# Performance work log

Measured on AMD Instinct MI355X. Metric: run time of the kernel, lower is better.

Reference implementation:

```python
import jax, jax.numpy as jnp
import numpy as np

H = 512; W = 512          # image size
K = 1024                  # fixed cap on points per cloud (original is data-dependent)
P = 8                     # n_points = n_points_rate * radius
R = 1.0                   # radius
THR = 5                   # point_threshould
LAM = 0.1                 # lam


def _lbp_uniform(img):
    """skimage-style uniform LBP, P=8, R=1, bilinear sampling (edge-clamped)."""
    Hh, Ww = img.shape
    rows = jnp.arange(Hh)
    cols = jnp.arange(Ww)
    bits = []
    for k in range(P):
        dr = float(np.round(-R * np.sin(2.0 * np.pi * k / P), 8))
        dc = float(np.round(R * np.cos(2.0 * np.pi * k / P), 8))
        rr = rows + dr
        cc = cols + dc
        r0 = jnp.floor(rr)
        c0 = jnp.floor(cc)
        fr = (rr - r0)[:, None]
        fc = (cc - c0)[None, :]
        r0i = jnp.clip(r0.astype(jnp.int32), 0, Hh - 1)
        r1i = jnp.clip(r0i + 1, 0, Hh - 1)
        c0i = jnp.clip(c0.astype(jnp.int32), 0, Ww - 1)
        c1i = jnp.clip(c0i + 1, 0, Ww - 1)
        g = lambda ri, ci: img[ri][:, ci]
        sample = ((1 - fr) * ((1 - fc) * g(r0i, c0i) + fc * g(r0i, c1i))
                  + fr * ((1 - fc) * g(r1i, c0i) + fc * g(r1i, c1i)))
        bits.append((sample - img >= 0).astype(jnp.int32))
    b = jnp.stack(bits)                                    # [P,H,W]
    changes = jnp.sum(jnp.abs(b - jnp.roll(b, 1, axis=0)), axis=0)
    s = jnp.sum(b, axis=0)
    return jnp.where(changes <= 2, s, P + 1).astype(jnp.float32)


def _select_points(mask2d):
    """Row-major coordinates of True pixels, zero-padded/truncated to K points."""
    flat = mask2d.reshape(-1)
    order = jnp.argsort(jnp.where(flat, 0, 1), stable=True)[:K]  # True pixels first, row-major
    valid = flat[order].astype(jnp.float32)
    r = (order // W).astype(jnp.float32)
    c = (order % W).astype(jnp.float32)
    return jnp.stack([r, c], axis=-1) * valid[:, None]     # [K,2]


def _pdist(x):
    sq = jnp.sum(x * x, axis=-1)
    d2 = sq[:, None] + sq[None, :] - 2.0 * (x @ x.T)
    return jnp.sqrt(jnp.maximum(d2, 0.0))


def _mst_pairing(D):
    """Prim's MST edges = dim-0 Vietoris-Rips persistence pairing. [K-1,2] int32."""
    N = D.shape[0]
    INF = jnp.float32(1e9)
    in_tree = jnp.zeros(N, bool).at[0].set(True)
    mind = D[0]
    src = jnp.zeros(N, jnp.int32)

    def step(carry, _):
        mind, src, in_tree = carry
        j = jnp.argmin(jnp.where(in_tree, INF, mind)).astype(jnp.int32)
        edge = jnp.stack([src[j], j])
        in_tree = in_tree.at[j].set(True)
        upd = (D[j] < mind) & ~in_tree
        mind = jnp.where(upd, D[j], mind)
        src = jnp.where(upd, j, src)
        return (mind, src, in_tree), edge

    _, edges = jax.lax.scan(step, (mind, src, in_tree), None, length=N - 1)
    return edges


def _sample_loss(pred_bin, mask_bin):
    pts_p = _select_points(_lbp_uniform(pred_bin) < THR)
    pts_m = _select_points(_lbp_uniform(mask_bin) < THR)
    Dp = _pdist(pts_p)
    Dm = _pdist(pts_m)
    ep = _mst_pairing(Dp)
    em = _mst_pairing(Dm)
    sig = lambda D, e: D[e[:, 0], e[:, 1]]
    l_p = jnp.linalg.norm(sig(Dp, ep) - sig(Dm, ep))   # signature of pred pairing
    l_m = jnp.linalg.norm(sig(Dp, em) - sig(Dm, em))   # signature of mask pairing
    return l_p + l_m


def setup_inputs() -> dict:
    key = jax.random.key(0)
    k1, k2, k3 = jax.random.split(key, 3)
    images = jax.random.normal(k1, (8, 1, H, W), dtype=jnp.float32)
    model_output = jax.random.normal(k2, (8, 1, H, W), dtype=jnp.float32)
    labels = jax.random.uniform(k3, (8, 1, H, W), dtype=jnp.float32)
    return {"images": images, "model_output": model_output, "labels": labels}


def reference(images, model_output, labels):
    preds = jax.nn.sigmoid(model_output[:, 0])          # squeeze channel dim
    masks = labels[:, 0]
    pred_bin = (preds > 0.5).astype(jnp.float32)
    mask_bin = (masks > 0.5).astype(jnp.float32)
    per_sample = jax.vmap(_sample_loss)(pred_bin, mask_bin)
    return LAM * jnp.sum(per_sample) / pred_bin.shape[0]
```

## Files before the change

kernel.cpp:

```cpp
#include <hip/hip_runtime.h>

#define HH 512
#define WW 512
#define NPIX (HH * WW)
#define NIMG 16
#define KPTS 1024
#define NWORDS (NPIX / 64)

__global__ void lbp_kernel(const float* __restrict__ mo,
                           const float* __restrict__ lb,
                           unsigned long long* __restrict__ maskbits) {
    int m = blockIdx.y;
    int pix = blockIdx.x * blockDim.x + threadIdx.x;
    int r = pix >> 9, c = pix & 511;
    int sample = m >> 1;
    const float* img = (m & 1) ? (lb + sample * NPIX) : (mo + sample * NPIX);
    float thr = (m & 1) ? 0.5f : 0.0f;

    int rm = r - (r > 0), rp = r + (r < HH - 1);
    int cm = c - (c > 0), cp = c + (c < WW - 1);
    const float* rowm = img + rm * WW;
    const float* row0 = img + r  * WW;
    const float* rowp = img + rp * WW;

    bool bmm = rowm[cm] > thr, bm0 = rowm[c] > thr, bmp = rowm[cp] > thr;
    bool b0m = row0[cm] > thr, b00 = row0[c] > thr, b0p = row0[cp] > thr;
    bool bpm = rowp[cm] > thr, bp0 = rowp[c] > thr, bpp = rowp[cp] > thr;

    bool r0e = (r == 0), c0e = (c == 0);
    bool t2m = r0e ? bpm : b0m;
    bool t2c = r0e ? bp0 : b00;
    bool t2p = r0e ? bpp : b0p;
    bool mc2 = c0e ? bmp : bm0;
    bool tc2 = c0e ? t2p : t2c;
    bool zc2 = c0e ? b0p : b00;
    bool pc2 = c0e ? bpp : bp0;

    unsigned bb =
        (b0p                     ?   1u : 0u)
      | ((bm0 & bmp & t2c & t2p) ?   2u : 0u)
      | (bm0                     ?   4u : 0u)
      | ((bmm & mc2 & t2m & tc2) ?   8u : 0u)
      | (b0m                     ?  16u : 0u)
      | ((b0m & zc2 & bpm & pc2) ?  32u : 0u)
      | (bp0                     ?  64u : 0u)
      | ((b0p & bp0 & bpp)       ? 128u : 0u);

    unsigned rol = ((bb << 1) | (bb >> 7)) & 0xFFu;
    int changes = __popc(bb ^ rol);
    int s = __popc(bb);
    bool maskbit = b00 && (changes <= 2) && (s < 5);

    unsigned long long w = __ballot(maskbit);
    if ((threadIdx.x & 63) == 0)
        maskbits[m * NWORDS + (pix >> 6)] = w;
}

__global__ void select_kernel(const unsigned long long* __restrict__ maskbits,
                              unsigned* __restrict__ ptsG) {
    __shared__ unsigned swv[4];
    int m = blockIdx.x, tid = threadIdx.x;
    int lane = tid & 63, wid = tid >> 6;

    for (int i = tid; i < KPTS; i += 256) ptsG[m * KPTS + i] = 0u;
    __syncthreads();

    unsigned running = 0;
    for (int ch = 0; ch < 16; ch++) {
        int w = ch * 256 + tid;
        unsigned long long word = maskbits[m * NWORDS + w];
        unsigned cnt = (unsigned)__popcll(word);

        unsigned x = cnt;
#pragma unroll
        for (int d = 1; d < 64; d <<= 1) {
            unsigned y = (unsigned)__shfl_up((int)x, d, 64);
            x += (lane >= d) ? y : 0u;
        }
        if (lane == 63) swv[wid] = x;
        __syncthreads();
        unsigned woff = 0, total = 0;
#pragma unroll
        for (int ww = 0; ww < 4; ww++) {
            unsigned t = swv[ww];
            total += t;
            woff += (ww < wid) ? t : 0u;
        }
        unsigned rank = running + woff + x - cnt;
        while (word) {
            int b = __builtin_ctzll(word);
            word &= word - 1;
            if (rank < (unsigned)KPTS) {
                unsigned p = (unsigned)(w * 64 + b);
                unsigned rr = p >> 9, cc = p & 511u;
                ptsG[m * KPTS + rank] = (rr << 16) | cc;
            }
            rank++;
        }
        running += total;
        if (running >= (unsigned)KPTS) break;
        __syncthreads();
    }
}

typedef short v2s __attribute__((ext_vector_type(2)));

__device__ __forceinline__ int dist2_packed(unsigned a, unsigned b) {
#if __has_builtin(__builtin_amdgcn_sdot2)
    v2s d = __builtin_bit_cast(v2s, a) - __builtin_bit_cast(v2s, b);
    return __builtin_amdgcn_sdot2(d, d, 0, false);
#else
    int dr = (int)(a >> 16) - (int)(b >> 16);
    int dc = (int)(a & 0xFFFFu) - (int)(b & 0xFFFFu);
    return __mul24(dr, dr) + __mul24(dc, dc);
#endif
}

template <int CTRL>
__device__ __forceinline__ unsigned umin_dpp(unsigned x) {
    unsigned o = (unsigned)__builtin_amdgcn_update_dpp((int)x, (int)x, CTRL,
                                                       0xf, 0xf, false);
    return o < x ? o : x;
}

__device__ __forceinline__ unsigned umin3(unsigned a, unsigned b, unsigned c) {
    unsigned t = a < b ? a : b;
    return t < c ? t : c;
}

__device__ __forceinline__ unsigned mk_key(unsigned ps, unsigned qs, int izb) {
#if __has_builtin(__builtin_amdgcn_sdot2)
    v2s d = __builtin_bit_cast(v2s, ps) - __builtin_bit_cast(v2s, qs);
    return (unsigned)__builtin_amdgcn_sdot2(d, d, izb, false);
#else
    int dr = (int)(short)(ps >> 16) - (int)(short)(qs >> 16);
    int dc = (int)(short)(ps & 0xFFFFu) - (int)(short)(qs & 0xFFFFu);
    return (unsigned)(dr * dr + dc * dc + izb);
#endif
}

#define SLOT_INIT(s, ps, ks, iz)                                          \
    iz = ((s << 6) | lane) - 1024;             \
    ps = base[(s << 6) | lane] << 5;             \
    ks = mk_key(ps, pt0s, iz);

#define SLOT_UPD(s, ps, ks, iz)                                           \
    { unsigned _nk = mk_key(ps, pjs, iz);                                 \
      ks = (unsigned)min((int)ks, (int)_nk); }

#define INLANE_MIN16(res)                                                 \
    { unsigned _m0 = umin3(k0, k1, k2);                                   \
      unsigned _m1 = umin3(k3, k4, k5);                                   \
      unsigned _m2 = umin3(k6, k7, k8);                                   \
      unsigned _m3 = umin3(k9, k10, k11);                                 \
      unsigned _m4 = umin3(k12, k13, k14);                                \
      unsigned _ra = umin3(_m0, _m1, _m2);                                \
      unsigned _rb = umin3(_m3, _m4, k15);                                \
      res = _ra < _rb ? _ra : _rb; }

#define SEL16P(res)                                                       \
    { unsigned _a0 = b0 ? p1  : p0;                                       \
      unsigned _a1 = b0 ? p3  : p2;                                       \
      unsigned _a2 = b0 ? p5  : p4;                                       \
      unsigned _a3 = b0 ? p7  : p6;                                       \
      unsigned _a4 = b0 ? p9  : p8;                                       \
      unsigned _a5 = b0 ? p11 : p10;                                      \
      unsigned _a6 = b0 ? p13 : p12;                                      \
      unsigned _a7 = b0 ? p15 : p14;                                      \
      unsigned _c0 = b1 ? _a1 : _a0;                                      \
      unsigned _c1 = b1 ? _a3 : _a2;                                      \
      unsigned _c2 = b1 ? _a5 : _a4;                                      \
      unsigned _c3 = b1 ? _a7 : _a6;                                      \
      unsigned _e0 = b2 ? _c1 : _c0;                                      \
      unsigned _e1 = b2 ? _c3 : _c2;                                      \
      res = b3 ? _e1 : _e0; }

#define PIN16(P) asm volatile("" :                                        \
    "+v"(P##0), "+v"(P##1), "+v"(P##2),  "+v"(P##3),                      \
    "+v"(P##4), "+v"(P##5), "+v"(P##6),  "+v"(P##7),                      \
    "+v"(P##8), "+v"(P##9), "+v"(P##10), "+v"(P##11),                     \
    "+v"(P##12), "+v"(P##13), "+v"(P##14), "+v"(P##15))

__global__ __launch_bounds__(64, 1) void mst_kernel(const unsigned* __restrict__ ptsG,
                                                    unsigned* __restrict__ edgesG) {
    int lane = threadIdx.x;
    int m = blockIdx.x;
    const unsigned* base = ptsG + m * KPTS;
    unsigned pt0s = base[0] << 5;

    unsigned k0,k1,k2,k3,k4,k5,k6,k7,k8,k9,k10,k11,k12,k13,k14,k15;
    unsigned p0,p1,p2,p3,p4,p5,p6,p7,p8,p9,p10,p11,p12,p13,p14,p15;
    int      i0,i1,i2,i3,i4,i5,i6,i7,i8,i9,i10,i11,i12,i13,i14,i15;

    SLOT_INIT(0,  p0,  k0,  i0);   SLOT_INIT(1,  p1,  k1,  i1);
    SLOT_INIT(2,  p2,  k2,  i2);   SLOT_INIT(3,  p3,  k3,  i3);
    SLOT_INIT(4,  p4,  k4,  i4);   SLOT_INIT(5,  p5,  k5,  i5);
    SLOT_INIT(6,  p6,  k6,  i6);   SLOT_INIT(7,  p7,  k7,  i7);
    SLOT_INIT(8,  p8,  k8,  i8);   SLOT_INIT(9,  p9,  k9,  i9);
    SLOT_INIT(10, p10, k10, i10);  SLOT_INIT(11, p11, k11, i11);
    SLOT_INIT(12, p12, k12, i12);  SLOT_INIT(13, p13, k13, i13);
    SLOT_INIT(14, p14, k14, i14);  SLOT_INIT(15, p15, k15, i15);

    unsigned* eout = edgesG + m * KPTS;
    unsigned rk;
    INLANE_MIN16(rk);

    unsigned acc = 0;

    for (int chk = 0; chk < 16; chk++) {
        int tmax = (chk < 15) ? 64 : 63;
        for (int t = 0; t < tmax; t++) {
            PIN16(p); PIN16(k);

            rk = umin_dpp<0x111>(rk);
            rk = umin_dpp<0x112>(rk);
            rk = umin_dpp<0x114>(rk);
            rk = umin_dpp<0x118>(rk);
            unsigned q0 = (unsigned)__builtin_amdgcn_readlane((int)rk, 15);
            unsigned q1 = (unsigned)__builtin_amdgcn_readlane((int)rk, 31);
            unsigned q2 = (unsigned)__builtin_amdgcn_readlane((int)rk, 47);
            unsigned q3 = (unsigned)__builtin_amdgcn_readlane((int)rk, 63);
            unsigned wa = q0 < q1 ? q0 : q1;
            unsigned wb = q2 < q3 ? q2 : q3;
            unsigned wk = (wa < wb ? wa : wb) + 1024u;

            unsigned j = wk & 1023u;
            int wslot = (int)(j >> 6);
            int wlane = (int)(j & 63u);

            bool b0 = (wslot & 1) != 0, b1 = (wslot & 2) != 0;
            bool b2 = (wslot & 4) != 0, b3 = (wslot & 8) != 0;
            unsigned selPay;
            SEL16P(selPay);
            unsigned pjs = (unsigned)__builtin_amdgcn_readlane((int)selPay, wlane);

            acc = (lane == t) ? wk : acc;

            SLOT_UPD(0,  p0,  k0,  i0);   SLOT_UPD(1,  p1,  k1,  i1);
            SLOT_UPD(2,  p2,  k2,  i2);   SLOT_UPD(3,  p3,  k3,  i3);
            SLOT_UPD(4,  p4,  k4,  i4);   SLOT_UPD(5,  p5,  k5,  i5);
            SLOT_UPD(6,  p6,  k6,  i6);   SLOT_UPD(7,  p7,  k7,  i7);
            SLOT_UPD(8,  p8,  k8,  i8);   SLOT_UPD(9,  p9,  k9,  i9);
            SLOT_UPD(10, p10, k10, i10);  SLOT_UPD(11, p11, k11, i11);
            SLOT_UPD(12, p12, k12, i12);  SLOT_UPD(13, p13, k13, i13);
            SLOT_UPD(14, p14, k14, i14);  SLOT_UPD(15, p15, k15, i15);

            INLANE_MIN16(rk);
        }
        eout[(chk << 6) + lane] = acc;
    }
}

__global__ void recover_kernel(const unsigned* __restrict__ ptsG,
                               const unsigned* __restrict__ edgesG,
                               float* __restrict__ contrib) {
    __shared__ unsigned sS[KPTS];
    __shared__ unsigned sO[KPTS];
    __shared__ unsigned short sT[KPTS];
    int g = blockIdx.x, m = blockIdx.y;
    int tid = threadIdx.x;
    int partner = m ^ 1;

    for (int i = tid; i < KPTS; i += 256) {
        sS[i] = ptsG[m * KPTS + i];
        sO[i] = ptsG[partner * KPTS + i];
    }
    for (int e = tid; e < KPTS - 1; e += 256) {
        unsigned wkk = edgesG[m * KPTS + e];
        sT[wkk & 1023u] = (unsigned short)(e + 1);
    }
    if (tid == 0) sT[0] = 0;
    __syncthreads();

    int lane = tid & 63, w = tid >> 6;
    for (int k = 0; k < 16; k++) {
        int e = g * 64 + w * 16 + k;
        if (e >= KPTS - 1) break;
        unsigned wk = edgesG[m * KPTS + e];
        unsigned j = wk & 1023u;
        unsigned d2p = wk >> 10;
        unsigned pj = sS[j];
        unsigned te1 = (unsigned)(e + 1);

        unsigned best = 0xFFFFFFFFu;
#pragma unroll
        for (int i = 0; i < 16; i++) {
            int v = i * 64 + lane;
            unsigned pv = sS[v];
            int d2 = dist2_packed(pv, pj);
            unsigned tv1 = (unsigned)sT[v];
            bool qual = ((unsigned)d2 == d2p) && (tv1 < te1);
            unsigned cand = qual ? ((tv1 << 10) | (unsigned)v) : 0xFFFFFFFFu;
            best = cand < best ? cand : best;
        }
#pragma unroll
        for (int dd = 32; dd; dd >>= 1) {
            unsigned o = (unsigned)__shfl_xor((int)best, dd, 64);
            best = o < best ? o : best;
        }
        unsigned vsrc = best & 1023u;
        if (lane == 0) {
            unsigned oj = sO[j], os = sO[vsrc];
            float Dp = __fsqrt_rn((float)d2p);
            float Dm = __fsqrt_rn((float)dist2_packed(oj, os));
            float diff = Dp - Dm;
            contrib[m * (KPTS - 1) + e] = diff * diff;
        }
    }
}

__global__ void final_kernel(const float* __restrict__ contrib,
                             float* __restrict__ out) {
    __shared__ double part[NIMG];
    int t = threadIdx.x;
    if (t < NIMG) {
        double s = 0.0;
        for (int e = 0; e < KPTS - 1; e++)
            s += (double)contrib[t * (KPTS - 1) + e];
        part[t] = sqrt(s);
    }
    __syncthreads();
    if (t == 0) {
        double tot = 0.0;
        for (int i = 0; i < NIMG; i++) tot += part[i];
        out[0] = (float)(0.1 * tot / 8.0);
    }
}

extern "C" void kernel_launch(void* const* d_in, const int* in_sizes, int n_in,
                              void* d_out, int out_size, void* d_ws, size_t ws_size,
                              hipStream_t stream) {
    const float* mo = (const float*)d_in[1];
    const float* lb = (const float*)d_in[2];

    unsigned long long* maskbits = (unsigned long long*)d_ws;
    unsigned* edgesG = (unsigned*)d_ws;
    float* contrib = (float*)((char*)d_ws + (size_t)64 * 1024);
    unsigned* ptsG = (unsigned*)((char*)d_ws + (size_t)NIMG * NWORDS * 8);
    float* out = (float*)d_out;

    lbp_kernel<<<dim3(NPIX / 256, NIMG), 256, 0, stream>>>(mo, lb, maskbits);
    select_kernel<<<NIMG, 256, 0, stream>>>(maskbits, ptsG);
    mst_kernel<<<NIMG, 64, 0, stream>>>(ptsG, edgesG);
    recover_kernel<<<dim3(16, NIMG), 256, 0, stream>>>(ptsG, edgesG, contrib);
    final_kernel<<<1, 64, 0, stream>>>(contrib, out);
}
```

Before: 435.1 us.

## Split Prim MST update across four waves with LDS cross-wave min

The Prim MST kernel now runs each cloud with 256 threads (four waves) instead of one wave. Each wave owns 4 of the 16 key slots, reduces them to lane 63 with DPP, and publishes the result to a double-buffered shared array; after a barrier every wave reads the four partials and takes the global min. Every wave still holds all 16 point payloads so it can look up the winner locally. This shortens the per-iteration distance-update work per wave, at the cost of a __syncthreads and an LDS round trip on each of the 1023 serial steps.

```diff
diff --git a/kernel.cpp b/kernel.cpp
--- a/kernel.cpp
+++ b/kernel.cpp
@@ -104,6 +104,7 @@
 }
 
 typedef short v2s __attribute__((ext_vector_type(2)));
+typedef unsigned u32x4 __attribute__((ext_vector_type(4)));
 
 __device__ __forceinline__ int dist2_packed(unsigned a, unsigned b) {
 #if __has_builtin(__builtin_amdgcn_sdot2)
@@ -123,6 +124,16 @@
     return o < x ? o : x;
 }
 
+__device__ __forceinline__ unsigned wave_min_to_lane63(unsigned x) {
+    x = umin_dpp<0x111>(x);
+    x = umin_dpp<0x112>(x);
+    x = umin_dpp<0x114>(x);
+    x = umin_dpp<0x118>(x);
+    x = umin_dpp<0x142>(x);
+    x = umin_dpp<0x143>(x);
+    return x;
+}
+
 __device__ __forceinline__ unsigned umin3(unsigned a, unsigned b, unsigned c) {
     unsigned t = a < b ? a : b;
     return t < c ? t : c;
@@ -139,24 +150,14 @@
 #endif
 }
 
-#define SLOT_INIT(s, ps, ks, iz)                                          \
-    iz = ((s << 6) | lane) - 1024;             \
-    ps = base[(s << 6) | lane] << 5;             \
-    ks = mk_key(ps, pt0s, iz);
-
-#define SLOT_UPD(s, ps, ks, iz)                                           \
-    { unsigned _nk = mk_key(ps, pjs, iz);                                 \
-      ks = (unsigned)min((int)ks, (int)_nk); }
-
-#define INLANE_MIN16(res)                                                 \
-    { unsigned _m0 = umin3(k0, k1, k2);                                   \
-      unsigned _m1 = umin3(k3, k4, k5);                                   \
-      unsigned _m2 = umin3(k6, k7, k8);                                   \
-      unsigned _m3 = umin3(k9, k10, k11);                                 \
-      unsigned _m4 = umin3(k12, k13, k14);                                \
-      unsigned _ra = umin3(_m0, _m1, _m2);                                \
-      unsigned _rb = umin3(_m3, _m4, k15);                                \
-      res = _ra < _rb ? _ra : _rb; }
+#define OSLOT_INIT(sl)                                                    \
+    oi##sl = (((wid * 4 + sl) << 6) | lane) - 1024;       \
+    oq##sl = base[((wid * 4 + sl) << 6) | lane] << 5;                     \
+    ok##sl = mk_key(oq##sl, pt0s, oi##sl);
+
+#define OSLOT_UPD(sl)                                                     \
+    { unsigned _nk = mk_key(oq##sl, pjs, oi##sl);                         \
+      ok##sl = (unsigned)min((int)ok##sl, (int)_nk); }
 
 #define SEL16P(res)                                                       \
     { unsigned _a0 = b0 ? p1  : p0;                                       \
@@ -175,54 +176,56 @@
       unsigned _e1 = b2 ? _c3 : _c2;                                      \
       res = b3 ? _e1 : _e0; }
 
-#define PIN16(P) asm volatile("" :                                        \
-    "+v"(P##0), "+v"(P##1), "+v"(P##2),  "+v"(P##3),                      \
-    "+v"(P##4), "+v"(P##5), "+v"(P##6),  "+v"(P##7),                      \
-    "+v"(P##8), "+v"(P##9), "+v"(P##10), "+v"(P##11),                     \
-    "+v"(P##12), "+v"(P##13), "+v"(P##14), "+v"(P##15))
-
-__global__ __launch_bounds__(64, 1) void mst_kernel(const unsigned* __restrict__ ptsG,
-                                                    unsigned* __restrict__ edgesG) {
-    int lane = threadIdx.x;
+__global__ __launch_bounds__(256, 1) void mst_kernel(const unsigned* __restrict__ ptsG,
+                                                     unsigned* __restrict__ edgesG) {
+    __shared__ __align__(16) unsigned xmin[2][4];
+    int tid = threadIdx.x;
+    int lane = tid & 63, wid = tid >> 6;
     int m = blockIdx.x;
     const unsigned* base = ptsG + m * KPTS;
     unsigned pt0s = base[0] << 5;
 
-    unsigned k0,k1,k2,k3,k4,k5,k6,k7,k8,k9,k10,k11,k12,k13,k14,k15;
-    unsigned p0,p1,p2,p3,p4,p5,p6,p7,p8,p9,p10,p11,p12,p13,p14,p15;
-    int      i0,i1,i2,i3,i4,i5,i6,i7,i8,i9,i10,i11,i12,i13,i14,i15;
-
-    SLOT_INIT(0,  p0,  k0,  i0);   SLOT_INIT(1,  p1,  k1,  i1);
-    SLOT_INIT(2,  p2,  k2,  i2);   SLOT_INIT(3,  p3,  k3,  i3);
-    SLOT_INIT(4,  p4,  k4,  i4);   SLOT_INIT(5,  p5,  k5,  i5);
-    SLOT_INIT(6,  p6,  k6,  i6);   SLOT_INIT(7,  p7,  k7,  i7);
-    SLOT_INIT(8,  p8,  k8,  i8);   SLOT_INIT(9,  p9,  k9,  i9);
-    SLOT_INIT(10, p10, k10, i10);  SLOT_INIT(11, p11, k11, i11);
-    SLOT_INIT(12, p12, k12, i12);  SLOT_INIT(13, p13, k13, i13);
-    SLOT_INIT(14, p14, k14, i14);  SLOT_INIT(15, p15, k15, i15);
+    unsigned p0  = base[( 0 << 6) | lane] << 5;
+    unsigned p1  = base[( 1 << 6) | lane] << 5;
+    unsigned p2  = base[( 2 << 6) | lane] << 5;
+    unsigned p3  = base[( 3 << 6) | lane] << 5;
+    unsigned p4  = base[( 4 << 6) | lane] << 5;
+    unsigned p5  = base[( 5 << 6) | lane] << 5;
+    unsigned p6  = base[( 6 << 6) | lane] << 5;
+    unsigned p7  = base[( 7 << 6) | lane] << 5;
+    unsigned p8  = base[( 8 << 6) | lane] << 5;
+    unsigned p9  = base[( 9 << 6) | lane] << 5;
+    unsigned p10 = base[(10 << 6) | lane] << 5;
+    unsigned p11 = base[(11 << 6) | lane] << 5;
+    unsigned p12 = base[(12 << 6) | lane] << 5;
+    unsigned p13 = base[(13 << 6) | lane] << 5;
+    unsigned p14 = base[(14 << 6) | lane] << 5;
+    unsigned p15 = base[(15 << 6) | lane] << 5;
+
+    unsigned oq0, oq1, oq2, oq3;
+    unsigned ok0, ok1, ok2, ok3;
+    int      oi0, oi1, oi2, oi3;
+    OSLOT_INIT(0); OSLOT_INIT(1); OSLOT_INIT(2); OSLOT_INIT(3);
 
     unsigned* eout = edgesG + m * KPTS;
-    unsigned rk;
-    INLANE_MIN16(rk);
+    unsigned r3i = umin3(ok0, ok1, ok2);
+    unsigned rk = r3i < ok3 ? r3i : ok3;
 
     unsigned acc = 0;
+    int par = 0;
 
     for (int chk = 0; chk < 16; chk++) {
         int tmax = (chk < 15) ? 64 : 63;
         for (int t = 0; t < tmax; t++) {
-            PIN16(p); PIN16(k);
-
-            rk = umin_dpp<0x111>(rk);
-            rk = umin_dpp<0x112>(rk);
-            rk = umin_dpp<0x114>(rk);
-            rk = umin_dpp<0x118>(rk);
-            unsigned q0 = (unsigned)__builtin_amdgcn_readlane((int)rk, 15);
-            unsigned q1 = (unsigned)__builtin_amdgcn_readlane((int)rk, 31);
-            unsigned q2 = (unsigned)__builtin_amdgcn_readlane((int)rk, 47);
-            unsigned q3 = (unsigned)__builtin_amdgcn_readlane((int)rk, 63);
-            unsigned wa = q0 < q1 ? q0 : q1;
-            unsigned wb = q2 < q3 ? q2 : q3;
-            unsigned wk = (wa < wb ? wa : wb) + 1024u;
+            unsigned wmin = wave_min_to_lane63(rk);
+            if (lane == 63) xmin[par][wid] = wmin;
+            __syncthreads();
+
+            u32x4 xv = *reinterpret_cast<const u32x4*>(&xmin[par][0]);
+            unsigned vm = umin3(xv.x, xv.y, xv.z);
+            vm = vm < xv.w ? vm : xv.w;
+            unsigned wk = (unsigned)__builtin_amdgcn_readfirstlane((int)vm) + 1024u;
+            par ^= 1;
 
             unsigned j = wk & 1023u;
             int wslot = (int)(j >> 6);
@@ -236,18 +239,11 @@
 
             acc = (lane == t) ? wk : acc;
 
-            SLOT_UPD(0,  p0,  k0,  i0);   SLOT_UPD(1,  p1,  k1,  i1);
-            SLOT_UPD(2,  p2,  k2,  i2);   SLOT_UPD(3,  p3,  k3,  i3);
-            SLOT_UPD(4,  p4,  k4,  i4);   SLOT_UPD(5,  p5,  k5,  i5);
-            SLOT_UPD(6,  p6,  k6,  i6);   SLOT_UPD(7,  p7,  k7,  i7);
-            SLOT_UPD(8,  p8,  k8,  i8);   SLOT_UPD(9,  p9,  k9,  i9);
-            SLOT_UPD(10, p10, k10, i10);  SLOT_UPD(11, p11, k11, i11);
-            SLOT_UPD(12, p12, k12, i12);  SLOT_UPD(13, p13, k13, i13);
-            SLOT_UPD(14, p14, k14, i14);  SLOT_UPD(15, p15, k15, i15);
-
-            INLANE_MIN16(rk);
-        }
-        eout[(chk << 6) + lane] = acc;
+            OSLOT_UPD(0); OSLOT_UPD(1); OSLOT_UPD(2); OSLOT_UPD(3);
+            unsigned r3 = umin3(ok0, ok1, ok2);
+            rk = r3 < ok3 ? r3 : ok3;
+        }
+        if (wid == 0) eout[(chk << 6) + lane] = acc;
     }
 }
 
@@ -341,7 +337,7 @@
 
     lbp_kernel<<<dim3(NPIX / 256, NIMG), 256, 0, stream>>>(mo, lb, maskbits);
     select_kernel<<<NIMG, 256, 0, stream>>>(maskbits, ptsG);
-    mst_kernel<<<NIMG, 64, 0, stream>>>(ptsG, edgesG);
+    mst_kernel<<<NIMG, 256, 0, stream>>>(ptsG, edgesG);
     recover_kernel<<<dim3(16, NIMG), 256, 0, stream>>>(ptsG, edgesG, contrib);
     final_kernel<<<1, 64, 0, stream>>>(contrib, out);
 }
```

New measurement: 412.2 us. -5.3%, faster.

## Interleave two independent Prim MST chains per wavefront to hide latency

Applied to the files above, without the earlier changes.

The MST kernel now processes two point clouds per 64-lane wavefront, interleaving their serial Prim iterations so the DPP reductions, readlanes and key updates of one chain can fill the latency gaps of the other. The grid is halved from 16 to 8 blocks, and the asm register pins are dropped in favour of unroll-1 loops. This trades fewer busy CUs and twice the registers per wave for more instruction-level parallelism in a latency-bound serial loop.

```diff
diff --git a/kernel.cpp b/kernel.cpp
--- a/kernel.cpp
+++ b/kernel.cpp
@@ -116,16 +116,16 @@
 #endif
 }
 
+__device__ __forceinline__ unsigned umin3(unsigned a, unsigned b, unsigned c) {
+    unsigned t = a < b ? a : b;
+    return t < c ? t : c;
+}
+
 template <int CTRL>
 __device__ __forceinline__ unsigned umin_dpp(unsigned x) {
     unsigned o = (unsigned)__builtin_amdgcn_update_dpp((int)x, (int)x, CTRL,
                                                        0xf, 0xf, false);
     return o < x ? o : x;
-}
-
-__device__ __forceinline__ unsigned umin3(unsigned a, unsigned b, unsigned c) {
-    unsigned t = a < b ? a : b;
-    return t < c ? t : c;
 }
 
 __device__ __forceinline__ unsigned mk_key(unsigned ps, unsigned qs, int izb) {
@@ -139,115 +139,126 @@
 #endif
 }
 
-#define SLOT_INIT(s, ps, ks, iz)                                          \
-    iz = ((s << 6) | lane) - 1024;             \
-    ps = base[(s << 6) | lane] << 5;             \
-    ks = mk_key(ps, pt0s, iz);
-
-#define SLOT_UPD(s, ps, ks, iz)                                           \
-    { unsigned _nk = mk_key(ps, pjs, iz);                                 \
-      ks = (unsigned)min((int)ks, (int)_nk); }
-
-#define INLANE_MIN16(res)                                                 \
-    { unsigned _m0 = umin3(k0, k1, k2);                                   \
-      unsigned _m1 = umin3(k3, k4, k5);                                   \
-      unsigned _m2 = umin3(k6, k7, k8);                                   \
-      unsigned _m3 = umin3(k9, k10, k11);                                 \
-      unsigned _m4 = umin3(k12, k13, k14);                                \
+#define SEL16B(P, B0, B1, B2, B3, res)                                    \
+    { unsigned _a0 = B0 ? P##1  : P##0;                                   \
+      unsigned _a1 = B0 ? P##3  : P##2;                                   \
+      unsigned _a2 = B0 ? P##5  : P##4;                                   \
+      unsigned _a3 = B0 ? P##7  : P##6;                                   \
+      unsigned _a4 = B0 ? P##9  : P##8;                                   \
+      unsigned _a5 = B0 ? P##11 : P##10;                                  \
+      unsigned _a6 = B0 ? P##13 : P##12;                                  \
+      unsigned _a7 = B0 ? P##15 : P##14;                                  \
+      unsigned _c0 = B1 ? _a1 : _a0;                                      \
+      unsigned _c1 = B1 ? _a3 : _a2;                                      \
+      unsigned _c2 = B1 ? _a5 : _a4;                                      \
+      unsigned _c3 = B1 ? _a7 : _a6;                                      \
+      unsigned _e0 = B2 ? _c1 : _c0;                                      \
+      unsigned _e1 = B2 ? _c3 : _c2;                                      \
+      res = B3 ? _e1 : _e0; }
+
+#define SLOT_INIT2(s)                                                     \
+    iz##s = ((s << 6) | lane) - 1024;                                     \
+    pX##s = baseX[(s << 6) | lane] << 5;                                  \
+    kX##s = mk_key(pX##s, pt0sX, iz##s);                                  \
+    pY##s = baseY[(s << 6) | lane] << 5;                                  \
+    kY##s = mk_key(pY##s, pt0sY, iz##s);
+
+#define UPD2(s)                                                           \
+    { unsigned _nX = mk_key(pX##s, pjsX, iz##s);                          \
+      kX##s = (unsigned)min((int)kX##s, (int)_nX);                        \
+      unsigned _nY = mk_key(pY##s, pjsY, iz##s);                          \
+      kY##s = (unsigned)min((int)kY##s, (int)_nY); }
+
+#define MIN16(K, res)                                                     \
+    { unsigned _m0 = umin3(K##0, K##1, K##2);                             \
+      unsigned _m1 = umin3(K##3, K##4, K##5);                             \
+      unsigned _m2 = umin3(K##6, K##7, K##8);                             \
+      unsigned _m3 = umin3(K##9, K##10, K##11);                           \
+      unsigned _m4 = umin3(K##12, K##13, K##14);                          \
       unsigned _ra = umin3(_m0, _m1, _m2);                                \
-      unsigned _rb = umin3(_m3, _m4, k15);                                \
+      unsigned _rb = umin3(_m3, _m4, K##15);                              \
       res = _ra < _rb ? _ra : _rb; }
-
-#define SEL16P(res)                                                       \
-    { unsigned _a0 = b0 ? p1  : p0;                                       \
-      unsigned _a1 = b0 ? p3  : p2;                                       \
-      unsigned _a2 = b0 ? p5  : p4;                                       \
-      unsigned _a3 = b0 ? p7  : p6;                                       \
-      unsigned _a4 = b0 ? p9  : p8;                                       \
-      unsigned _a5 = b0 ? p11 : p10;                                      \
-      unsigned _a6 = b0 ? p13 : p12;                                      \
-      unsigned _a7 = b0 ? p15 : p14;                                      \
-      unsigned _c0 = b1 ? _a1 : _a0;                                      \
-      unsigned _c1 = b1 ? _a3 : _a2;                                      \
-      unsigned _c2 = b1 ? _a5 : _a4;                                      \
-      unsigned _c3 = b1 ? _a7 : _a6;                                      \
-      unsigned _e0 = b2 ? _c1 : _c0;                                      \
-      unsigned _e1 = b2 ? _c3 : _c2;                                      \
-      res = b3 ? _e1 : _e0; }
-
-#define PIN16(P) asm volatile("" :                                        \
-    "+v"(P##0), "+v"(P##1), "+v"(P##2),  "+v"(P##3),                      \
-    "+v"(P##4), "+v"(P##5), "+v"(P##6),  "+v"(P##7),                      \
-    "+v"(P##8), "+v"(P##9), "+v"(P##10), "+v"(P##11),                     \
-    "+v"(P##12), "+v"(P##13), "+v"(P##14), "+v"(P##15))
 
 __global__ __launch_bounds__(64, 1) void mst_kernel(const unsigned* __restrict__ ptsG,
                                                     unsigned* __restrict__ edgesG) {
     int lane = threadIdx.x;
-    int m = blockIdx.x;
-    const unsigned* base = ptsG + m * KPTS;
-    unsigned pt0s = base[0] << 5;
-
-    unsigned k0,k1,k2,k3,k4,k5,k6,k7,k8,k9,k10,k11,k12,k13,k14,k15;
-    unsigned p0,p1,p2,p3,p4,p5,p6,p7,p8,p9,p10,p11,p12,p13,p14,p15;
-    int      i0,i1,i2,i3,i4,i5,i6,i7,i8,i9,i10,i11,i12,i13,i14,i15;
-
-    SLOT_INIT(0,  p0,  k0,  i0);   SLOT_INIT(1,  p1,  k1,  i1);
-    SLOT_INIT(2,  p2,  k2,  i2);   SLOT_INIT(3,  p3,  k3,  i3);
-    SLOT_INIT(4,  p4,  k4,  i4);   SLOT_INIT(5,  p5,  k5,  i5);
-    SLOT_INIT(6,  p6,  k6,  i6);   SLOT_INIT(7,  p7,  k7,  i7);
-    SLOT_INIT(8,  p8,  k8,  i8);   SLOT_INIT(9,  p9,  k9,  i9);
-    SLOT_INIT(10, p10, k10, i10);  SLOT_INIT(11, p11, k11, i11);
-    SLOT_INIT(12, p12, k12, i12);  SLOT_INIT(13, p13, k13, i13);
-    SLOT_INIT(14, p14, k14, i14);  SLOT_INIT(15, p15, k15, i15);
-
-    unsigned* eout = edgesG + m * KPTS;
-    unsigned rk;
-    INLANE_MIN16(rk);
-
-    unsigned acc = 0;
-
+    int b = blockIdx.x;
+    const unsigned* baseX = ptsG + (2 * b)     * KPTS;
+    const unsigned* baseY = ptsG + (2 * b + 1) * KPTS;
+    unsigned pt0sX = baseX[0] << 5;
+    unsigned pt0sY = baseY[0] << 5;
+
+    unsigned pX0,pX1,pX2,pX3,pX4,pX5,pX6,pX7,pX8,pX9,pX10,pX11,pX12,pX13,pX14,pX15;
+    unsigned pY0,pY1,pY2,pY3,pY4,pY5,pY6,pY7,pY8,pY9,pY10,pY11,pY12,pY13,pY14,pY15;
+    unsigned kX0,kX1,kX2,kX3,kX4,kX5,kX6,kX7,kX8,kX9,kX10,kX11,kX12,kX13,kX14,kX15;
+    unsigned kY0,kY1,kY2,kY3,kY4,kY5,kY6,kY7,kY8,kY9,kY10,kY11,kY12,kY13,kY14,kY15;
+    int      iz0,iz1,iz2,iz3,iz4,iz5,iz6,iz7,iz8,iz9,iz10,iz11,iz12,iz13,iz14,iz15;
+
+    SLOT_INIT2(0)  SLOT_INIT2(1)  SLOT_INIT2(2)  SLOT_INIT2(3)
+    SLOT_INIT2(4)  SLOT_INIT2(5)  SLOT_INIT2(6)  SLOT_INIT2(7)
+    SLOT_INIT2(8)  SLOT_INIT2(9)  SLOT_INIT2(10) SLOT_INIT2(11)
+    SLOT_INIT2(12) SLOT_INIT2(13) SLOT_INIT2(14) SLOT_INIT2(15)
+
+    unsigned* eoutX = edgesG + (2 * b)     * KPTS;
+    unsigned* eoutY = edgesG + (2 * b + 1) * KPTS;
+
+    unsigned rX, rY;
+    MIN16(kX, rX);
+    MIN16(kY, rY);
+
+    unsigned accX = 0, accY = 0;
+
+#pragma unroll 1
     for (int chk = 0; chk < 16; chk++) {
         int tmax = (chk < 15) ? 64 : 63;
+#pragma unroll 1
         for (int t = 0; t < tmax; t++) {
-            PIN16(p); PIN16(k);
-
-            rk = umin_dpp<0x111>(rk);
-            rk = umin_dpp<0x112>(rk);
-            rk = umin_dpp<0x114>(rk);
-            rk = umin_dpp<0x118>(rk);
-            unsigned q0 = (unsigned)__builtin_amdgcn_readlane((int)rk, 15);
-            unsigned q1 = (unsigned)__builtin_amdgcn_readlane((int)rk, 31);
-            unsigned q2 = (unsigned)__builtin_amdgcn_readlane((int)rk, 47);
-            unsigned q3 = (unsigned)__builtin_amdgcn_readlane((int)rk, 63);
-            unsigned wa = q0 < q1 ? q0 : q1;
-            unsigned wb = q2 < q3 ? q2 : q3;
-            unsigned wk = (wa < wb ? wa : wb) + 1024u;
-
-            unsigned j = wk & 1023u;
-            int wslot = (int)(j >> 6);
-            int wlane = (int)(j & 63u);
-
-            bool b0 = (wslot & 1) != 0, b1 = (wslot & 2) != 0;
-            bool b2 = (wslot & 4) != 0, b3 = (wslot & 8) != 0;
-            unsigned selPay;
-            SEL16P(selPay);
-            unsigned pjs = (unsigned)__builtin_amdgcn_readlane((int)selPay, wlane);
-
-            acc = (lane == t) ? wk : acc;
-
-            SLOT_UPD(0,  p0,  k0,  i0);   SLOT_UPD(1,  p1,  k1,  i1);
-            SLOT_UPD(2,  p2,  k2,  i2);   SLOT_UPD(3,  p3,  k3,  i3);
-            SLOT_UPD(4,  p4,  k4,  i4);   SLOT_UPD(5,  p5,  k5,  i5);
-            SLOT_UPD(6,  p6,  k6,  i6);   SLOT_UPD(7,  p7,  k7,  i7);
-            SLOT_UPD(8,  p8,  k8,  i8);   SLOT_UPD(9,  p9,  k9,  i9);
-            SLOT_UPD(10, p10, k10, i10);  SLOT_UPD(11, p11, k11, i11);
-            SLOT_UPD(12, p12, k12, i12);  SLOT_UPD(13, p13, k13, i13);
-            SLOT_UPD(14, p14, k14, i14);  SLOT_UPD(15, p15, k15, i15);
-
-            INLANE_MIN16(rk);
-        }
-        eout[(chk << 6) + lane] = acc;
+            rX = umin_dpp<0x111>(rX);  rY = umin_dpp<0x111>(rY);
+            rX = umin_dpp<0x112>(rX);  rY = umin_dpp<0x112>(rY);
+            rX = umin_dpp<0x114>(rX);  rY = umin_dpp<0x114>(rY);
+            rX = umin_dpp<0x118>(rX);  rY = umin_dpp<0x118>(rY);
+            unsigned q0X = (unsigned)__builtin_amdgcn_readlane((int)rX, 15);
+            unsigned q0Y = (unsigned)__builtin_amdgcn_readlane((int)rY, 15);
+            unsigned q1X = (unsigned)__builtin_amdgcn_readlane((int)rX, 31);
+            unsigned q1Y = (unsigned)__builtin_amdgcn_readlane((int)rY, 31);
+            unsigned q2X = (unsigned)__builtin_amdgcn_readlane((int)rX, 47);
+            unsigned q2Y = (unsigned)__builtin_amdgcn_readlane((int)rY, 47);
+            unsigned q3X = (unsigned)__builtin_amdgcn_readlane((int)rX, 63);
+            unsigned q3Y = (unsigned)__builtin_amdgcn_readlane((int)rY, 63);
+            unsigned waX = q0X < q1X ? q0X : q1X;
+            unsigned waY = q0Y < q1Y ? q0Y : q1Y;
+            unsigned wbX = q2X < q3X ? q2X : q3X;
+            unsigned wbY = q2Y < q3Y ? q2Y : q3Y;
+            unsigned wkX = (waX < wbX ? waX : wbX) + 1024u;
+            unsigned wkY = (waY < wbY ? waY : wbY) + 1024u;
+
+            unsigned jX = wkX & 1023u, jY = wkY & 1023u;
+            int wsX = (int)(jX >> 6), wlX = (int)(jX & 63u);
+            int wsY = (int)(jY >> 6), wlY = (int)(jY & 63u);
+
+            bool bX0 = (wsX & 1) != 0, bX1 = (wsX & 2) != 0;
+            bool bX2 = (wsX & 4) != 0, bX3 = (wsX & 8) != 0;
+            bool bY0 = (wsY & 1) != 0, bY1 = (wsY & 2) != 0;
+            bool bY2 = (wsY & 4) != 0, bY3 = (wsY & 8) != 0;
+            unsigned selX, selY;
+            SEL16B(pX, bX0, bX1, bX2, bX3, selX);
+            SEL16B(pY, bY0, bY1, bY2, bY3, selY);
+            unsigned pjsX = (unsigned)__builtin_amdgcn_readlane((int)selX, wlX);
+            unsigned pjsY = (unsigned)__builtin_amdgcn_readlane((int)selY, wlY);
+
+            accX = (lane == t) ? wkX : accX;
+            accY = (lane == t) ? wkY : accY;
+
+            UPD2(0)  UPD2(1)  UPD2(2)  UPD2(3)
+            UPD2(4)  UPD2(5)  UPD2(6)  UPD2(7)
+            UPD2(8)  UPD2(9)  UPD2(10) UPD2(11)
+            UPD2(12) UPD2(13) UPD2(14) UPD2(15)
+
+            MIN16(kX, rX);
+            MIN16(kY, rY);
+        }
+        eoutX[(chk << 6) + lane] = accX;
+        eoutY[(chk << 6) + lane] = accY;
     }
 }
 
@@ -341,7 +352,7 @@
 
     lbp_kernel<<<dim3(NPIX / 256, NIMG), 256, 0, stream>>>(mo, lb, maskbits);
     select_kernel<<<NIMG, 256, 0, stream>>>(maskbits, ptsG);
-    mst_kernel<<<NIMG, 64, 0, stream>>>(ptsG, edgesG);
+    mst_kernel<<<NIMG / 2, 64, 0, stream>>>(ptsG, edgesG);
     recover_kernel<<<dim3(16, NIMG), 256, 0, stream>>>(ptsG, edgesG, contrib);
     final_kernel<<<1, 64, 0, stream>>>(contrib, out);
 }
```

Measured after the change: 698.2 us. +60.5%, slower.
